# Optimization experiments

Measured on AMD Instinct MI355X. Metric: run time of the kernel, lower is better.

The kernel has to match this reference:

```python
import jax, jax.numpy as jnp
import numpy as np

N, E, DIN, H, M, O = 100000, 3200000, 128, 256, 500, 100


def setup_inputs() -> dict:
    key = jax.random.key(0)
    ks = jax.random.split(key, 8)
    x = jax.random.normal(ks[0], (N, DIN), dtype=jnp.float32)
    edge_index = jax.random.randint(ks[1], (2, E), 0, N, dtype=jnp.int64)
    # GCNConv weights (glorot-ish scale) and biases
    W1 = jax.random.normal(ks[2], (DIN, H), dtype=jnp.float32) / np.sqrt(DIN)
    b1 = jnp.zeros((H,), dtype=jnp.float32)
    W2 = jax.random.normal(ks[3], (H, M), dtype=jnp.float32) / np.sqrt(H)
    b2 = jnp.zeros((M,), dtype=jnp.float32)
    # output head ('GO'): Linear(M -> O)
    Wout = jax.random.normal(ks[4], (M, O), dtype=jnp.float32) / np.sqrt(M)
    bout = jnp.zeros((O,), dtype=jnp.float32)
    # threshold param stored as inv_softplus(1.0) so softplus(threshold)=1.0
    threshold = jnp.float32(np.log(np.expm1(1.0)))
    return {"x": x, "edge_index": edge_index, "W1": W1, "b1": b1,
            "W2": W2, "b2": b2, "Wout": Wout, "bout": bout,
            "threshold": threshold}


def reference(x, edge_index, W1, b1, W2, b2, Wout, bout, threshold):
    src, dst = edge_index[0], edge_index[1]
    n = x.shape[0]
    # GCN sym-normalization with improved=True (self-loop weight 2):
    # deg[i] = 2 + #incoming edges; norm(e) = deg^-1/2[src] * deg^-1/2[dst]
    deg = jax.ops.segment_sum(jnp.ones(src.shape[0], x.dtype), dst,
                              num_segments=n) + jnp.asarray(2.0, x.dtype)
    dinv = jax.lax.rsqrt(deg)
    coef = dinv[src] * dinv[dst]              # [E]
    self_coef = (2.0 * dinv * dinv)[:, None]  # [N,1] self-loop term

    def gcn_conv(h, W, b):
        h = h @ W                              # [N,C]
        agg = jax.ops.segment_sum(h[src] * coef[:, None], dst, num_segments=n)
        return agg + self_coef * h + b

    h = jax.nn.relu(gcn_conv(x, W1, b1))       # conv + ReLU (no bn, no dropout)
    module_representation = jax.nn.softplus(gcn_conv(h, W2, b2))  # [N,M]
    # tanh probability transform: tanh(softplus(threshold) * x)
    p = jnp.tanh(jax.nn.softplus(threshold) * module_representation)
    y_go = p @ Wout + bout                     # output head 'GO'
    return (module_representation, y_go)
```

## Files before the change

### kernel.cpp

```cpp
#include <hip/hip_runtime.h>
#include <cstdint>
#include <cstddef>

#define DIN 128
#define HID 256
#define MODD 500
#define OUTD 100

typedef unsigned int uint;
typedef unsigned short ushort;
typedef __attribute__((ext_vector_type(8))) __bf16 bf16x8;
typedef __attribute__((ext_vector_type(4))) float f32x4;

__device__ __forceinline__ float bf2f(ushort u) {
    return __uint_as_float(((uint)u) << 16);
}
__device__ __forceinline__ ushort f2bf(float f) {
    uint u = __float_as_uint(f);
    return (ushort)((u + 0x7FFF + ((u >> 16) & 1)) >> 16);
}
__device__ __forceinline__ uint packbf2(float lo, float hi) {
    return (uint)f2bf(lo) | ((uint)f2bf(hi) << 16);
}
__device__ __forceinline__ void async_copy16(const void* g, void* l) {
    __builtin_amdgcn_global_load_lds((const __attribute__((address_space(1))) void*)g,
                                     (__attribute__((address_space(3))) void*)l, 16, 0, 0);
}
__device__ __forceinline__ float tanh_fast(float x) {
    return 1.0f - 2.0f / (__expf(2.0f * x) + 1.0f);
}
__device__ __forceinline__ float softplus_fast(float v) {
    return fmaxf(v, 0.0f) + __logf(1.0f + __expf(-fabsf(v)));
}
__device__ __forceinline__ void acc8(float* a, uint4 v, float w) {
    a[0] += w * bf2f((ushort)(v.x & 0xFFFF));
    a[1] += w * bf2f((ushort)(v.x >> 16));
    a[2] += w * bf2f((ushort)(v.y & 0xFFFF));
    a[3] += w * bf2f((ushort)(v.y >> 16));
    a[4] += w * bf2f((ushort)(v.z & 0xFFFF));
    a[5] += w * bf2f((ushort)(v.z >> 16));
    a[6] += w * bf2f((ushort)(v.w & 0xFFFF));
    a[7] += w * bf2f((ushort)(v.w >> 16));
}


#define BSH 9
#define MAXB 256
#define PCH 8192

__global__ __launch_bounds__(256)
void bucket_count(const int* __restrict__ dst, int* __restrict__ btot, int E, int NB) {
    __shared__ int hist[MAXB];
    int tid = threadIdx.x;
    int e0 = blockIdx.x * PCH;
    int e1 = min(e0 + PCH, E);
    for (int b = tid; b < MAXB; b += 256) hist[b] = 0;
    __syncthreads();
    for (int e = e0 + tid; e < e1; e += 256)
        atomicAdd(&hist[dst[e] >> BSH], 1);
    __syncthreads();
    for (int b = tid; b < NB; b += 256)
        if (hist[b]) atomicAdd(&btot[b], hist[b]);
}

__global__ void scan_buckets(const int* __restrict__ btot, int* __restrict__ bstart,
                             int* __restrict__ bcur, int* __restrict__ rp,
                             int NB, int N, int E) {
    if (threadIdx.x == 0 && blockIdx.x == 0) {
        int s = 0;
        for (int b = 0; b < NB; ++b) { bstart[b] = s; bcur[b] = s; s += btot[b]; }
        bstart[NB] = s;
        rp[N] = E;
    }
}

__global__ __launch_bounds__(256)
void partition_edges(const int* __restrict__ src, const int* __restrict__ dst,
                     int* __restrict__ bcur, uint* __restrict__ pairBuf,
                     int E, int NB) {
    __shared__ int hist[MAXB];
    __shared__ int gbase[MAXB];
    int tid = threadIdx.x;
    int e0 = blockIdx.x * PCH;
    int e1 = min(e0 + PCH, E);
    for (int b = tid; b < NB; b += 256) hist[b] = 0;
    __syncthreads();
    for (int e = e0 + tid; e < e1; e += 256) {
        int d = dst[e];
        atomicAdd(&hist[d >> BSH], 1);
    }
    __syncthreads();
    for (int b = tid; b < NB; b += 256) {
        int h = hist[b];
        gbase[b] = h ? atomicAdd(&bcur[b], h) : 0;
        hist[b] = 0;
    }
    __syncthreads();
    for (int e = e0 + tid; e < e1; e += 256) {
        int d = dst[e];
        int s = src[e];
        int b = d >> BSH;
        int idx = gbase[b] + atomicAdd(&hist[b], 1);
        pairBuf[idx] = (uint)s | ((uint)(d & ((1 << BSH) - 1)) << 20);
    }
}

__global__ __launch_bounds__(512)
void bucket_scatter(const uint* __restrict__ pairBuf, const int* __restrict__ bstart,
                    int* __restrict__ col, int* __restrict__ rp,
                    float* __restrict__ dinv, int N) {
    __shared__ int lcnt[1 << BSH];
    __shared__ int lcur[1 << BSH];
    __shared__ int wsum[8];
    int tid = threadIdx.x;
    int lane = tid & 63;
    int w = tid >> 6;
    int b = blockIdx.x;
    int n0 = b << BSH;
    int nn = min(1 << BSH, N - n0);
    int start = bstart[b];
    int end = bstart[b + 1];

    lcnt[tid] = 0;
    __syncthreads();
    for (int e = start + tid; e < end; e += 512)
        atomicAdd(&lcnt[pairBuf[e] >> 20], 1);
    __syncthreads();
    int cnt = lcnt[tid];
    int x = cnt;
    #pragma unroll
    for (int off = 1; off < 64; off <<= 1) {
        int t = __shfl_up(x, off);
        if (lane >= off) x += t;
    }
    if (lane == 63) wsum[w] = x;
    __syncthreads();
    if (tid == 0) {
        int s = 0;
        #pragma unroll
        for (int k = 0; k < 8; ++k) { int t = wsum[k]; wsum[k] = s; s += t; }
    }
    __syncthreads();
    int excl = start + wsum[w] + (x - cnt);
    if (tid < nn) {
        rp[n0 + tid] = excl;
        dinv[n0 + tid] = rsqrtf((float)cnt + 2.0f);
    }
    lcur[tid] = excl;
    __syncthreads();
    for (int e = start + tid; e < end; e += 512) {
        uint v = pairBuf[e];
        int pos = atomicAdd(&lcur[v >> 20], 1);
        col[pos] = (int)(v & 0xFFFFF);
    }
}


__global__ void cast_f32_bf16(const float* __restrict__ src, ushort* __restrict__ dst, int n4) {
    int i = blockIdx.x * blockDim.x + threadIdx.x;
    if (i < n4) {
        float4 v = ((const float4*)src)[i];
        ushort4 o;
        o.x = f2bf(v.x); o.y = f2bf(v.y); o.z = f2bf(v.z); o.w = f2bf(v.w);
        ((ushort4*)dst)[i] = o;
    }
}

__global__ void transpose_cast(const float* __restrict__ src, ushort* __restrict__ dst,
                               int K, int N, int Kpad, int Npad) {
    int idx = blockIdx.x * blockDim.x + threadIdx.x;
    if (idx >= Npad * Kpad) return;
    int n = idx / Kpad, k = idx - n * Kpad;
    float v = (n < N && k < K) ? src[(size_t)k * N + n] : 0.0f;
    dst[idx] = f2bf(v);
}


__global__ void aggregate128(const ushort* __restrict__ X, ushort* __restrict__ Y,
                             const int* __restrict__ rp, const int* __restrict__ col,
                             const float* __restrict__ dinv, int N) {
    int gw = blockIdx.x * (blockDim.x >> 6) + (threadIdx.x >> 6);
    int lane = threadIdx.x & 63;
    if (gw >= N) return;
    int g = lane >> 4;
    int sub = lane & 15;
    float di = dinv[gw];
    float sc = 2.0f * di * di;
    const uint4* Xr = (const uint4*)X;
    float a[8] = {};
    if (g == 0) acc8(a, Xr[(size_t)gw * 16 + sub], sc);
    int e = rp[gw], end = rp[gw + 1];
    int base = e;
    for (; base + 8 <= end; base += 8) {
        int c0 = col[base + g];
        int c1 = col[base + 4 + g];
        float w0 = dinv[c0] * di, w1 = dinv[c1] * di;
        uint4 v0 = Xr[(size_t)c0 * 16 + sub];
        uint4 v1 = Xr[(size_t)c1 * 16 + sub];
        acc8(a, v0, w0);
        acc8(a, v1, w1);
    }
    if (base + 4 <= end) {
        int c0 = col[base + g];
        float w0 = dinv[c0] * di;
        acc8(a, Xr[(size_t)c0 * 16 + sub], w0);
        base += 4;
    }
    int rem = end - base;
    if (g < rem) {
        int c0 = col[base + g];
        float w0 = dinv[c0] * di;
        acc8(a, Xr[(size_t)c0 * 16 + sub], w0);
    }
    #pragma unroll
    for (int q = 0; q < 8; ++q) {
        a[q] += __shfl_xor(a[q], 16);
        a[q] += __shfl_xor(a[q], 32);
    }
    if (g == 0) {
        uint4 o;
        o.x = packbf2(a[0], a[1]);
        o.y = packbf2(a[2], a[3]);
        o.z = packbf2(a[4], a[5]);
        o.w = packbf2(a[6], a[7]);
        ((uint4*)Y)[(size_t)gw * 16 + sub] = o;
    }
}

__global__ void aggregate256(const ushort* __restrict__ X, ushort* __restrict__ Y,
                             const int* __restrict__ rp, const int* __restrict__ col,
                             const float* __restrict__ dinv, int N) {
    int gw = blockIdx.x * (blockDim.x >> 6) + (threadIdx.x >> 6);
    int lane = threadIdx.x & 63;
    if (gw >= N) return;
    int g = lane >> 5;
    int sub = lane & 31;
    float di = dinv[gw];
    float sc = 2.0f * di * di;
    const uint4* Xr = (const uint4*)X;
    float a[8] = {};
    if (g == 0) acc8(a, Xr[(size_t)gw * 32 + sub], sc);
    int e = rp[gw], end = rp[gw + 1];
    int base = e;
    for (; base + 4 <= end; base += 4) {
        int c0 = col[base + g];
        int c1 = col[base + 2 + g];
        float w0 = dinv[c0] * di, w1 = dinv[c1] * di;
        uint4 v0 = Xr[(size_t)c0 * 32 + sub];
        uint4 v1 = Xr[(size_t)c1 * 32 + sub];
        acc8(a, v0, w0);
        acc8(a, v1, w1);
    }
    if (base + 2 <= end) {
        int c0 = col[base + g];
        float w0 = dinv[c0] * di;
        acc8(a, Xr[(size_t)c0 * 32 + sub], w0);
        base += 2;
    }
    if (base < end && g == 0) {
        int c0 = col[base];
        float w0 = dinv[c0] * di;
        acc8(a, Xr[(size_t)c0 * 32 + sub], w0);
    }
    #pragma unroll
    for (int q = 0; q < 8; ++q) a[q] += __shfl_xor(a[q], 32);
    if (g == 0) {
        uint4 o;
        o.x = packbf2(a[0], a[1]);
        o.y = packbf2(a[2], a[3]);
        o.z = packbf2(a[4], a[5]);
        o.w = packbf2(a[6], a[7]);
        ((uint4*)Y)[(size_t)gw * 32 + sub] = o;
    }
}


template<int K, int MODE>
__global__ __launch_bounds__(512)
void gemm_wide(const ushort* __restrict__ A, const ushort* __restrict__ BT,
               const float* __restrict__ bias, void* __restrict__ Cout,
               int M, int Nact, int ldc, ushort* __restrict__ C2,
               const float* __restrict__ thr) {
    __shared__ ushort sA[128 * 32];
    __shared__ ushort sB[256 * 32];
    int tid = threadIdx.x;
    int lane = tid & 63;
    int w = tid >> 6;
    int wr = w >> 2, wc = w & 3;
    int row0 = blockIdx.y * 128;
    int col0 = blockIdx.x * 256;
    float sp = 0.0f;
    if (MODE == 3) sp = softplus_fast(*thr);
    f32x4 acc[4][4] = {};

    for (int kt = 0; kt < K; kt += 32) {
        if (kt) __syncthreads();
        {
            int r = tid >> 2;
            int ko = (tid & 3) * 8;
            int rr = min(row0 + r, M - 1);
            async_copy16(A + (size_t)rr * K + kt + ko, sA + (size_t)tid * 8);
        }
        #pragma unroll
        for (int L = 0; L < 2; ++L) {
            int c = L * 512 + tid;
            int nr = c >> 2;
            int ko = (c & 3) * 8;
            async_copy16(BT + (size_t)(col0 + nr) * K + kt + ko, sB + (size_t)c * 8);
        }
        __syncthreads();
        bf16x8 af[4], bfr[4];
        #pragma unroll
        for (int i = 0; i < 4; ++i) {
            int row = wr * 64 + i * 16 + (lane & 15);
            af[i] = *(const bf16x8*)(sA + row * 32 + (lane >> 4) * 8);
        }
        #pragma unroll
        for (int j = 0; j < 4; ++j) {
            int n = wc * 64 + j * 16 + (lane & 15);
            bfr[j] = *(const bf16x8*)(sB + n * 32 + (lane >> 4) * 8);
        }
        #pragma unroll
        for (int i = 0; i < 4; ++i)
            #pragma unroll
            for (int j = 0; j < 4; ++j)
                acc[i][j] = __builtin_amdgcn_mfma_f32_16x16x32_bf16(af[i], bfr[j], acc[i][j], 0, 0, 0);
    }

    #pragma unroll
    for (int i = 0; i < 4; ++i) {
        #pragma unroll
        for (int j = 0; j < 4; ++j) {
            int col = col0 + wc * 64 + j * 16 + (lane & 15);
            if (MODE == 3) {
                bool act = (col < Nact);
                float bv = act ? bias[col] : 0.0f;
                #pragma unroll
                for (int r = 0; r < 4; ++r) {
                    int row = row0 + wr * 64 + i * 16 + (lane >> 4) * 4 + r;
                    if (row >= M) continue;
                    if (act) {
                        float v = softplus_fast(acc[i][j][r] + bv);
                        ((float*)Cout)[(size_t)row * ldc + col] = v;
                        C2[(size_t)row * 512 + col] = f2bf(tanh_fast(sp * v));
                    } else {
                        C2[(size_t)row * 512 + col] = 0;
                    }
                }
            } else {
                if (col >= Nact) continue;
                float bv = bias[col];
                #pragma unroll
                for (int r = 0; r < 4; ++r) {
                    int row = row0 + wr * 64 + i * 16 + (lane >> 4) * 4 + r;
                    if (row >= M) continue;
                    float v = acc[i][j][r] + bv;
                    if (MODE == 0) {
                        v = fmaxf(v, 0.0f);
                        ((ushort*)Cout)[(size_t)row * ldc + col] = f2bf(v);
                    } else {
                        ((float*)Cout)[(size_t)row * ldc + col] = v;
                    }
                }
            }
        }
    }
}

template<int K, int MODE>
__global__ __launch_bounds__(256)
void gemm_bt(const ushort* __restrict__ A, const ushort* __restrict__ BT,
             const float* __restrict__ bias, void* __restrict__ Cout,
             int M, int Nact, int ldc) {
    __shared__ ushort sA[128 * 32];
    __shared__ ushort sB[128 * 32];
    int tid = threadIdx.x;
    int lane = tid & 63;
    int w = tid >> 6;
    int wr = w >> 1, wc = w & 1;
    int row0 = blockIdx.y * 128;
    int col0 = blockIdx.x * 128;
    f32x4 acc[4][4] = {};

    for (int kt = 0; kt < K; kt += 32) {
        if (kt) __syncthreads();
        #pragma unroll
        for (int L = 0; L < 2; ++L) {
            int cb = L * 256 + w * 64;
            int c = cb + lane;
            int r = c >> 2;
            int ko = (c & 3) * 8;
            int rr = min(row0 + r, M - 1);
            async_copy16(A + (size_t)rr * K + kt + ko, sA + (size_t)cb * 8);
        }
        #pragma unroll
        for (int L = 0; L < 2; ++L) {
            int cb = L * 256 + w * 64;
            int c = cb + lane;
            int nr = c >> 2;
            int ko = (c & 3) * 8;
            async_copy16(BT + (size_t)(col0 + nr) * K + kt + ko, sB + (size_t)cb * 8);
        }
        __syncthreads();
        bf16x8 af[4], bfr[4];
        #pragma unroll
        for (int i = 0; i < 4; ++i) {
            int row = wr * 64 + i * 16 + (lane & 15);
            af[i] = *(const bf16x8*)(sA + row * 32 + (lane >> 4) * 8);
        }
        #pragma unroll
        for (int j = 0; j < 4; ++j) {
            int n = wc * 64 + j * 16 + (lane & 15);
            bfr[j] = *(const bf16x8*)(sB + n * 32 + (lane >> 4) * 8);
        }
        #pragma unroll
        for (int i = 0; i < 4; ++i)
            #pragma unroll
            for (int j = 0; j < 4; ++j)
                acc[i][j] = __builtin_amdgcn_mfma_f32_16x16x32_bf16(af[i], bfr[j], acc[i][j], 0, 0, 0);
    }

    #pragma unroll
    for (int i = 0; i < 4; ++i) {
        #pragma unroll
        for (int j = 0; j < 4; ++j) {
            int col = col0 + wc * 64 + j * 16 + (lane & 15);
            if (col >= Nact) continue;
            float bv = bias[col];
            #pragma unroll
            for (int r = 0; r < 4; ++r) {
                int row = row0 + wr * 64 + i * 16 + (lane >> 4) * 4 + r;
                if (row >= M) continue;
                float v = acc[i][j][r] + bv;
                if (MODE == 0) {
                    v = fmaxf(v, 0.0f);
                    ((ushort*)Cout)[(size_t)row * ldc + col] = f2bf(v);
                } else {
                    ((float*)Cout)[(size_t)row * ldc + col] = v;
                }
            }
        }
    }
}


extern "C" void kernel_launch(void* const* d_in, const int* in_sizes, int n_in,
                              void* d_out, int out_size, void* d_ws, size_t ws_size,
                              hipStream_t stream) {
    const float* x    = (const float*)d_in[0];
    const int*   ei   = (const int*)d_in[1];
    const float* W1   = (const float*)d_in[2];
    const float* b1   = (const float*)d_in[3];
    const float* W2   = (const float*)d_in[4];
    const float* b2   = (const float*)d_in[5];
    const float* Wout = (const float*)d_in[6];
    const float* bout = (const float*)d_in[7];
    const float* thr  = (const float*)d_in[8];

    int N = in_sizes[0] / DIN;
    int E = in_sizes[1] / 2;
    const int* srcI = ei;
    const int* dstI = ei + E;

    char* wsp = (char*)d_ws;
    size_t o = 0;
    auto alloc = [&](size_t bytes) -> void* {
        void* p = wsp + o;
        o = (o + bytes + 255) & ~(size_t)255;
        return p;
    };
    float*  dinv   = (float*)alloc((size_t)N * 4);
    int*    rp     = (int*)alloc((size_t)(N + 1) * 4);
    int*    btot   = (int*)alloc(MAXB * 4);
    int*    bstart = (int*)alloc((MAXB + 1) * 4);
    int*    bcur   = (int*)alloc(MAXB * 4);
    ushort* W1T    = (ushort*)alloc((size_t)256 * 128 * 2);
    ushort* W2T    = (ushort*)alloc((size_t)512 * 256 * 2);
    ushort* WoutT  = (ushort*)alloc((size_t)128 * 512 * 2);
    ushort* bufA   = (ushort*)alloc((size_t)N * 256 * 2);
    size_t  col_off = o;
    int*    col   = (int*)alloc((size_t)E * 4);
    ushort* hbuf  = (ushort*)alloc((size_t)N * 256 * 2);
    size_t  pbf_need = col_off + (size_t)N * 512 * 2;
    if (o < pbf_need) o = (pbf_need + 255) & ~(size_t)255;
    ushort* pbf = (ushort*)(wsp + col_off);

    ushort* xbf = bufA;
    ushort* xa  = bufA + (size_t)N * 128;
    ushort* ha  = bufA;
    uint* pairBuf = (uint*)hbuf;

    float* mr   = (float*)d_out;
    float* yout = (float*)d_out + (size_t)N * MODD;

    int mtiles = (N + 127) / 128;
    int NB = (N + (1 << BSH) - 1) >> BSH;

    hipMemsetAsync(btot, 0, (size_t)NB * 4, stream);
    bucket_count<<<(E + PCH - 1) / PCH, 256, 0, stream>>>(dstI, btot, E, NB);
    scan_buckets<<<1, 64, 0, stream>>>(btot, bstart, bcur, rp, NB, N, E);
    partition_edges<<<(E + PCH - 1) / PCH, 256, 0, stream>>>(srcI, dstI, bcur, pairBuf, E, NB);
    bucket_scatter<<<NB, 512, 0, stream>>>(pairBuf, bstart, col, rp, dinv, N);

    cast_f32_bf16<<<((N * DIN / 4) + 255) / 256, 256, 0, stream>>>(x, xbf, N * DIN / 4);
    transpose_cast<<<(256 * 128 + 255) / 256, 256, 0, stream>>>(W1, W1T, 128, 256, 128, 256);
    transpose_cast<<<(512 * 256 + 255) / 256, 256, 0, stream>>>(W2, W2T, 256, 500, 256, 512);
    transpose_cast<<<(128 * 512 + 255) / 256, 256, 0, stream>>>(Wout, WoutT, 500, 100, 512, 128);

    aggregate128<<<(N + 3) / 4, 256, 0, stream>>>(xbf, xa, rp, col, dinv, N);
    gemm_wide<128, 0><<<dim3(1, mtiles), 512, 0, stream>>>(xa, W1T, b1, hbuf, N, HID, HID,
                                                           nullptr, nullptr);

    aggregate256<<<(N + 3) / 4, 256, 0, stream>>>(hbuf, ha, rp, col, dinv, N);
    gemm_wide<256, 3><<<dim3(2, mtiles), 512, 0, stream>>>(ha, W2T, b2, mr, N, MODD, MODD,
                                                           pbf, thr);

    gemm_bt<512, 2><<<dim3(1, mtiles), 256, 0, stream>>>(pbf, WoutT, bout, yout, N, OUTD, OUTD);
}
```

Baseline: 956.3 us.

## Split hidden features into two 128-wide halves for aggregation

The first GEMM now writes the 256-wide hidden activations as two separate N×128 planes. The second aggregation runs as two aggregate128 passes, one per plane, instead of a single aggregate256. The second GEMM reads its A operand from the two planes. This is meant to shrink the working set of each gather pass so neighbour rows stay in cache better, at the cost of reading the CSR structure twice and adding one extra kernel launch.

```diff
diff --git a/kernel.cpp b/kernel.cpp
--- a/kernel.cpp
+++ b/kernel.cpp
@@ -227,60 +227,13 @@
     }
 }
 
-__global__ void aggregate256(const ushort* __restrict__ X, ushort* __restrict__ Y,
-                             const int* __restrict__ rp, const int* __restrict__ col,
-                             const float* __restrict__ dinv, int N) {
-    int gw = blockIdx.x * (blockDim.x >> 6) + (threadIdx.x >> 6);
-    int lane = threadIdx.x & 63;
-    if (gw >= N) return;
-    int g = lane >> 5;
-    int sub = lane & 31;
-    float di = dinv[gw];
-    float sc = 2.0f * di * di;
-    const uint4* Xr = (const uint4*)X;
-    float a[8] = {};
-    if (g == 0) acc8(a, Xr[(size_t)gw * 32 + sub], sc);
-    int e = rp[gw], end = rp[gw + 1];
-    int base = e;
-    for (; base + 4 <= end; base += 4) {
-        int c0 = col[base + g];
-        int c1 = col[base + 2 + g];
-        float w0 = dinv[c0] * di, w1 = dinv[c1] * di;
-        uint4 v0 = Xr[(size_t)c0 * 32 + sub];
-        uint4 v1 = Xr[(size_t)c1 * 32 + sub];
-        acc8(a, v0, w0);
-        acc8(a, v1, w1);
-    }
-    if (base + 2 <= end) {
-        int c0 = col[base + g];
-        float w0 = dinv[c0] * di;
-        acc8(a, Xr[(size_t)c0 * 32 + sub], w0);
-        base += 2;
-    }
-    if (base < end && g == 0) {
-        int c0 = col[base];
-        float w0 = dinv[c0] * di;
-        acc8(a, Xr[(size_t)c0 * 32 + sub], w0);
-    }
-    #pragma unroll
-    for (int q = 0; q < 8; ++q) a[q] += __shfl_xor(a[q], 32);
-    if (g == 0) {
-        uint4 o;
-        o.x = packbf2(a[0], a[1]);
-        o.y = packbf2(a[2], a[3]);
-        o.z = packbf2(a[4], a[5]);
-        o.w = packbf2(a[6], a[7]);
-        ((uint4*)Y)[(size_t)gw * 32 + sub] = o;
-    }
-}
-
-
-template<int K, int MODE>
+
+template<int K, int MODE, bool SPLITA>
 __global__ __launch_bounds__(512)
-void gemm_wide(const ushort* __restrict__ A, const ushort* __restrict__ BT,
-               const float* __restrict__ bias, void* __restrict__ Cout,
-               int M, int Nact, int ldc, ushort* __restrict__ C2,
-               const float* __restrict__ thr) {
+void gemm_wide(const ushort* __restrict__ A, const ushort* __restrict__ A2,
+               const ushort* __restrict__ BT, const float* __restrict__ bias,
+               void* __restrict__ Cout, int M, int Nact, int ldc,
+               ushort* __restrict__ C2, const float* __restrict__ thr) {
     __shared__ ushort sA[128 * 32];
     __shared__ ushort sB[256 * 32];
     int tid = threadIdx.x;
@@ -299,7 +252,14 @@
             int r = tid >> 2;
             int ko = (tid & 3) * 8;
             int rr = min(row0 + r, M - 1);
-            async_copy16(A + (size_t)rr * K + kt + ko, sA + (size_t)tid * 8);
+            int k = kt + ko;
+            const ushort* srcp;
+            if (SPLITA)
+                srcp = (k < 128) ? (A + (size_t)rr * 128 + k)
+                                 : (A2 + (size_t)rr * 128 + (k - 128));
+            else
+                srcp = A + (size_t)rr * K + k;
+            async_copy16(srcp, sA + (size_t)tid * 8);
         }
         #pragma unroll
         for (int L = 0; L < 2; ++L) {
@@ -347,6 +307,18 @@
                         C2[(size_t)row * 512 + col] = 0;
                     }
                 }
+            } else if (MODE == 0) {
+                if (col >= Nact) continue;
+                float bv = bias[col];
+                ushort* dsth = (col < 128) ? (ushort*)Cout : C2;
+                int ch = col & 127;
+                #pragma unroll
+                for (int r = 0; r < 4; ++r) {
+                    int row = row0 + wr * 64 + i * 16 + (lane >> 4) * 4 + r;
+                    if (row >= M) continue;
+                    float v = fmaxf(acc[i][j][r] + bv, 0.0f);
+                    dsth[(size_t)row * 128 + ch] = f2bf(v);
+                }
             } else {
                 if (col >= Nact) continue;
                 float bv = bias[col];
@@ -354,13 +326,7 @@
                 for (int r = 0; r < 4; ++r) {
                     int row = row0 + wr * 64 + i * 16 + (lane >> 4) * 4 + r;
                     if (row >= M) continue;
-                    float v = acc[i][j][r] + bv;
-                    if (MODE == 0) {
-                        v = fmaxf(v, 0.0f);
-                        ((ushort*)Cout)[(size_t)row * ldc + col] = f2bf(v);
-                    } else {
-                        ((float*)Cout)[(size_t)row * ldc + col] = v;
-                    }
+                    ((float*)Cout)[(size_t)row * ldc + col] = acc[i][j][r] + bv;
                 }
             }
         }
@@ -487,7 +453,10 @@
 
     ushort* xbf = bufA;
     ushort* xa  = bufA + (size_t)N * 128;
-    ushort* ha  = bufA;
+    ushort* haA = bufA;
+    ushort* haB = bufA + (size_t)N * 128;
+    ushort* hA  = hbuf;
+    ushort* hB  = hbuf + (size_t)N * 128;
     uint* pairBuf = (uint*)hbuf;
 
     float* mr   = (float*)d_out;
@@ -508,12 +477,14 @@
     transpose_cast<<<(128 * 512 + 255) / 256, 256, 0, stream>>>(Wout, WoutT, 500, 100, 512, 128);
 
     aggregate128<<<(N + 3) / 4, 256, 0, stream>>>(xbf, xa, rp, col, dinv, N);
-    gemm_wide<128, 0><<<dim3(1, mtiles), 512, 0, stream>>>(xa, W1T, b1, hbuf, N, HID, HID,
-                                                           nullptr, nullptr);
-
-    aggregate256<<<(N + 3) / 4, 256, 0, stream>>>(hbuf, ha, rp, col, dinv, N);
-    gemm_wide<256, 3><<<dim3(2, mtiles), 512, 0, stream>>>(ha, W2T, b2, mr, N, MODD, MODD,
-                                                           pbf, thr);
+    gemm_wide<128, 0, false><<<dim3(1, mtiles), 512, 0, stream>>>(
+        xa, nullptr, W1T, b1, hA, N, HID, HID, hB, nullptr);
+
+    aggregate128<<<(N + 3) / 4, 256, 0, stream>>>(hA, haA, rp, col, dinv, N);
+    aggregate128<<<(N + 3) / 4, 256, 0, stream>>>(hB, haB, rp, col, dinv, N);
+
+    gemm_wide<256, 3, true><<<dim3(2, mtiles), 512, 0, stream>>>(
+        haA, haB, W2T, b2, mr, N, MODD, MODD, pbf, thr);
 
     gemm_bt<512, 2><<<dim3(1, mtiles), 256, 0, stream>>>(pbf, WoutT, bout, yout, N, OUTD, OUTD);
 }
```

Result: no change. 955.2 us (-0.1%).
